# Optimization experiments

Measured on AMD Instinct MI355X. Metric: run time of the kernel, lower is better.

## Reference

```python
import jax, jax.numpy as jnp
import numpy as np

NEG = -9e15
EPS = 1e-5

# GraphAttention (classic GAT layer): h = xW; e_ij = LeakyReLU(a1.h_i + a2.h_j);
# attention = softmax(where(adj>0, e, -9e15)); out = attention @ h.
# The torch code builds one big block-diagonal adjacency; off-block entries get
# -9e15 and underflow to exactly 0 after softmax, so batched per-block GAT is
# numerically identical and avoids the O((B*N)^2) dense waste.

def gat(x, adj, W, a1, a2):
    h = jnp.einsum('bnf,fh->bnh', x, W)
    e = jax.nn.leaky_relu(jnp.einsum('bnh,h->bn', h, a1)[:, :, None]
                          + jnp.einsum('bnh,h->bn', h, a2)[:, None, :], 0.2)
    att = jax.nn.softmax(jnp.where(adj > 0, e, NEG), axis=-1)
    return jnp.einsum('bnm,bmh->bnh', att, h)

def mlp(x, W1, b1, W2, b2):
    return jax.nn.relu(x @ W1 + b1) @ W2 + b2


def setup_inputs() -> dict:
    key = jax.random.key(0)
    ks = iter(jax.random.split(key, 40))
    B, NV, NO = 8, 500, 1500
    DV, DO, H = 512, 32, 128

    def mat(din, dout):
        return jax.random.normal(next(ks), (din, dout), jnp.float32) / np.sqrt(din)

    def vec(d):
        return jax.random.normal(next(ks), (d,), jnp.float32) * 0.1

    inp = {
        'vis_memory': jax.random.normal(next(ks), (B, NV, DV), jnp.float32),
        'obj_memory': jax.random.normal(next(ks), (B, NO, DO), jnp.float32),
        'vis_adj': jax.random.uniform(next(ks), (B, NV, NV), jnp.float32),
        'obj_adj': jax.random.uniform(next(ks), (B, NO, NO), jnp.float32),
        'object_A_OV': jax.random.uniform(next(ks), (B, NO, NV), jnp.float32),
        # GAT layers
        'Wv1': mat(DV, H), 'av1a': vec(H), 'av1b': vec(H),
        'Wv2': mat(H, H),  'av2a': vec(H), 'av2b': vec(H),
        'Wo1': mat(DO, H), 'ao1a': vec(H), 'ao1b': vec(H),
        'Wo2': mat(H, H),  'ao2a': vec(H), 'ao2b': vec(H),
        # globalTobject / objectTglobal MLPs
        'g2o_W1': mat(H, H), 'g2o_b1': jnp.zeros((H,), jnp.float32),
        'g2o_W2': mat(H, H), 'g2o_b2': jnp.zeros((H,), jnp.float32),
        'o2g_W1': mat(H, H), 'o2g_b1': jnp.zeros((H,), jnp.float32),
        'o2g_W2': mat(H, H), 'o2g_b2': jnp.zeros((H,), jnp.float32),
        # output projections
        'img_W': mat(H, DV), 'img_b': jnp.zeros((DV,), jnp.float32),
        'obj_W': mat(H, DO), 'obj_b': jnp.zeros((DO,), jnp.float32),
    }
    return inp


def reference(vis_memory, obj_memory, vis_adj, obj_adj, object_A_OV,
              Wv1, av1a, av1b, Wv2, av2a, av2b,
              Wo1, ao1a, ao1b, Wo2, ao2a, ao2b,
              g2o_W1, g2o_b1, g2o_W2, g2o_b2,
              o2g_W1, o2g_b1, o2g_W2, o2g_b2,
              img_W, img_b, obj_W, obj_b):
    # cross adjacencies (block-diagonal in torch -> batched here)
    vo = jnp.swapaxes(object_A_OV, 1, 2)            # (B, NV, NO)
    vo = vo / (vo.sum(2, keepdims=True) + EPS)
    ov = jnp.swapaxes(vo, 1, 2)                     # (B, NO, NV)
    ov = ov / (ov.sum(2, keepdims=True) + EPS)

    v1 = jax.nn.relu(gat(vis_memory, vis_adj, Wv1, av1a, av1b))
    o1 = jax.nn.relu(gat(obj_memory, obj_adj, Wo1, ao1a, ao1b))
    vis = v1 + mlp(jnp.einsum('bvo,boh->bvh', vo, o1), o2g_W1, o2g_b1, o2g_W2, o2g_b2)
    obj = o1 + mlp(jnp.einsum('bov,bvh->boh', ov, v1), g2o_W1, g2o_b1, g2o_W2, g2o_b2)

    v2 = jax.nn.relu(gat(vis, vis_adj, Wv2, av2a, av2b))
    o2 = jax.nn.relu(gat(obj, obj_adj, Wo2, ao2a, ao2b))
    vis = v2 + mlp(jnp.einsum('bvo,boh->bvh', vo, o2), o2g_W1, o2g_b1, o2g_W2, o2g_b2)
    obj = o2 + mlp(jnp.einsum('bov,bvh->boh', ov, v2), g2o_W1, g2o_b1, g2o_W2, g2o_b2)

    vis_out = vis @ img_W + img_b                   # (B, NV, DV)
    obj_out = obj @ obj_W + obj_b                   # (B, NO, DO)
    return (vis_out, obj_out)
```

## Files before the change

kernel.cpp:

```cpp
#include <hip/hip_runtime.h>
#include <math.h>

#define EPSV 1e-5f
#define HD 128
#define IT 64
#define JT 32
#define WP 68
#define CCH 16
#define THR 256

typedef __attribute__((address_space(3))) uint32_t lds_u32_t;
typedef __attribute__((address_space(1))) uint32_t gbl_u32_t;
typedef __attribute__((ext_vector_type(8))) short bf16x8;
typedef __attribute__((ext_vector_type(4))) float f32x4;

__device__ __forceinline__ void async_copy16(const float* g, float* l) {
    __builtin_amdgcn_global_load_lds((const gbl_u32_t*)g, (lds_u32_t*)l, 16, 0, 0);
}

__device__ __forceinline__ void stage_tile_async(const float* gsrc, float* lds, int t) {
    int wv = t >> 6, lane = t & 63;
#pragma unroll
    for (int it = 0; it < 4; ++it) {
        int c = it * 4 + wv;
        async_copy16(gsrc + c * 256 + lane * 4, lds + c * 256);
    }
}

__device__ __forceinline__ void stage_8k(const void* g, void* l, int t) {
    const float* gf = (const float*)g; float* lf = (float*)l;
    async_copy16(gf + t * 4, lf + t * 4);
    async_copy16(gf + t * 4 + 1024, lf + t * 4 + 1024);
}

__device__ __forceinline__ unsigned int f2bf(float f) {
    return __builtin_bit_cast(unsigned int, f) >> 16;
}

__device__ __forceinline__ unsigned short rne_bf16(float f) {
    unsigned int u = __builtin_bit_cast(unsigned int, f);
    u += 0x7FFFu + ((u >> 16) & 1u);
    return (unsigned short)(u >> 16);
}

struct WprepP { const float *W, *a1, *a2; unsigned short* WT; float *wa1, *wa2; int K; };
struct XprepP { const float* X; unsigned short* Xbf; const float *wa1, *wa2;
                float *sa, *sb; int rows; };
struct GmfP   { const unsigned short *Xbf, *WT; unsigned short* hT; int N, tilesJ; };
struct MaskP  { const float* adj; unsigned int* maskT; int N, tilesJ, chunks; };
struct AggP  { const unsigned int* mask; const float *sa, *sb, *sm; const unsigned short* hT;
               float *pp, *zp; int N, tiles, tilesJ, tps; };
struct CrossP{ const float *A, *src, *rs1; float *pp; int iN, jN, tiles, tps; };
struct FinP  { const float *pp, *zp; float *out; int rows, S; };
struct MlpP  { const float *pp, *scale; int S; const float *W1, *b1, *W2, *b2, *res;
               float *out; int rows; };


__global__ void colsum_part_k(const float* __restrict__ A, float* __restrict__ s1p,
                              int B, int NO, int NV) {
    int v = blockIdx.x * 256 + threadIdx.x;
    int c = blockIdx.y, b = blockIdx.z;
    if (v >= NV) return;
    int chunk = (NO + CCH - 1) / CCH;
    int o0 = c * chunk;
    int o1 = o0 + chunk; if (o1 > NO) o1 = NO;
    const float* Ab = A + (size_t)b * NO * NV + v;
    float s = 0.f;
    for (int o = o0; o < o1; ++o) s += Ab[(size_t)o * NV];
    s1p[((size_t)b * CCH + c) * NV + v] = s;
}

__global__ void colsum_fin_k(const float* __restrict__ s1p, float* __restrict__ rs1,
                             int B, int NV) {
    int idx = blockIdx.x * 256 + threadIdx.x;
    if (idx >= B * NV) return;
    int b = idx / NV, v = idx - b * NV;
    float s = 0.f;
    for (int c = 0; c < CCH; ++c) s += s1p[((size_t)b * CCH + c) * NV + v];
    rs1[idx] = 1.f / (s + EPSV);
}

__global__ void rowsum_inv_k(const float* __restrict__ A, const float* __restrict__ rs1,
                             float* __restrict__ rs2, int B, int NO, int NV) {
    int row = blockIdx.x * (blockDim.x >> 6) + (threadIdx.x >> 6);
    int lane = threadIdx.x & 63;
    if (row >= B * NO) return;
    int b = row / NO;
    const float* Ar = A + (size_t)row * NV;
    const float* r1 = rs1 + (size_t)b * NV;
    float s = 0.f;
    for (int v = lane; v < NV; v += 64) s += Ar[v] * r1[v];
    for (int off = 32; off; off >>= 1) s += __shfl_xor(s, off, 64);
    if (lane == 0) rs2[row] = 1.f / (s + EPSV);
}

__global__ __launch_bounds__(256)
void mask2_k(MaskP V, MaskP O, int GV) {
    int bid = blockIdx.x;
    const MaskP& P = (bid < GV) ? V : O;
    int lb = (bid < GV) ? bid : bid - GV;
    int t = threadIdx.x;
    int wid = lb * 4 + (t >> 6), lane = t & 63;
    int N = P.N, chunks = P.chunks, tilesJ = P.tilesJ;
    int row = wid / chunks;
    int ch = wid - row * chunks;
    if (row >= 8 * N) return;
    int b = row / N, i = row - b * N;
    int j = ch * 64 + lane;
    float v = (j < N) ? P.adj[(size_t)row * N + j] : 0.f;
    unsigned long long m = __ballot(v > 0.f);
    size_t base = (size_t)b * tilesJ * N;
    int w0 = ch * 2;
    if (lane == 0)                      P.maskT[base + (size_t)w0 * N + i] = (unsigned int)m;
    if (lane == 32 && w0 + 1 < tilesJ)  P.maskT[base + (size_t)(w0 + 1) * N + i] = (unsigned int)(m >> 32);
}

__global__ __launch_bounds__(256)
void wprep_k(WprepP p0, WprepP p1, WprepP p2, WprepP p3, int e0, int e1, int e2) {
    __shared__ float lw[32][129];
    __shared__ float a1s[128], a2s[128];
    int bid = blockIdx.x;
    const WprepP& P = bid < e0 ? p0 : bid < e1 ? p1 : bid < e2 ? p2 : p3;
    int lb = bid < e0 ? bid : bid < e1 ? bid - e0 : bid < e2 ? bid - e1 : bid - e2;
    int k0 = lb * 32, K = P.K;
    int t = threadIdx.x;
    if (t < 128) { a1s[t] = P.a1[t]; a2s[t] = P.a2[t]; }
    for (int idx = t; idx < 32 * 32; idx += 256) {
        int kk = idx >> 5, c4 = idx & 31;
        float4 v = ((const float4*)(P.W + (size_t)(k0 + kk) * 128))[c4];
        lw[kk][c4 * 4 + 0] = v.x; lw[kk][c4 * 4 + 1] = v.y;
        lw[kk][c4 * 4 + 2] = v.z; lw[kk][c4 * 4 + 3] = v.w;
    }
    __syncthreads();
    int kk = t >> 3, g = t & 7;
    float s1 = 0.f, s2 = 0.f;
    for (int c = g; c < 128; c += 8) {
        float w = lw[kk][c];
        s1 = fmaf(w, a1s[c], s1);
        s2 = fmaf(w, a2s[c], s2);
    }
    s1 += __shfl_xor(s1, 1, 64); s1 += __shfl_xor(s1, 2, 64); s1 += __shfl_xor(s1, 4, 64);
    s2 += __shfl_xor(s2, 1, 64); s2 += __shfl_xor(s2, 2, 64); s2 += __shfl_xor(s2, 4, 64);
    if (g == 0) { P.wa1[k0 + kk] = s1; P.wa2[k0 + kk] = s2; }
    for (int idx = t; idx < 4096; idx += 256) {
        int c = idx >> 5, k = idx & 31;
        P.WT[(size_t)c * K + k0 + k] = rne_bf16(lw[k][c]);
    }
}

template<int K>
__device__ void xprep_body(const XprepP& P, int lb) {
    int t = threadIdx.x, wv = t >> 6, lane = t & 63;
    int row = lb * 4 + wv;
    if (row >= P.rows) return;
    const float4* x4 = (const float4*)(P.X + (size_t)row * K);
    const float4* w14 = (const float4*)P.wa1;
    const float4* w24 = (const float4*)P.wa2;
    unsigned short* xb = P.Xbf + (size_t)row * K;
    float s1 = 0.f, s2 = 0.f;
    constexpr int K4 = K / 4;
    constexpr int NI = (K4 + 63) / 64;
#pragma unroll
    for (int i = 0; i < NI; ++i) {
        int k4 = i * 64 + lane;
        if ((K4 % 64 == 0) || (k4 < K4)) {
            float4 x = x4[k4];
            float4 a = w14[k4];
            float4 b = w24[k4];
            s1 += x.x * a.x + x.y * a.y + x.z * a.z + x.w * a.w;
            s2 += x.x * b.x + x.y * b.y + x.z * b.z + x.w * b.w;
            ushort4 p = make_ushort4(rne_bf16(x.x), rne_bf16(x.y),
                                     rne_bf16(x.z), rne_bf16(x.w));
            *(ushort4*)(xb + (size_t)k4 * 4) = p;
        }
    }
#pragma unroll
    for (int off = 32; off; off >>= 1) {
        s1 += __shfl_xor(s1, off, 64);
        s2 += __shfl_xor(s2, off, 64);
    }
    if (lane == 0) { P.sa[row] = s1; P.sb[row] = s2; }
}

template<int KV, int KO>
__global__ __launch_bounds__(256)
void xprep2_k(XprepP V, XprepP O, int GV) {
    int bid = blockIdx.x;
    if (bid < GV) xprep_body<KV>(V, bid);
    else          xprep_body<KO>(O, bid - GV);
}

template<int K>
__device__ void gmf_body(const GmfP& P, int lb) {
    int tilesJ = P.tilesJ, N = P.N;
    int b = lb / tilesJ, jt = lb - b * tilesJ;
    int t = threadIdx.x, wv = t >> 6, lane = t & 63;
    int ml = lane & 15, quad = lane >> 4;
    const unsigned short* xb = P.Xbf + ((size_t)b * N + (size_t)jt * 32) * K;
    const unsigned short* wt0 = P.WT + (size_t)(wv * 32 + ml) * K;
    const unsigned short* wt1 = wt0 + (size_t)16 * K;
    const unsigned short* xb0 = xb + (size_t)ml * K;
    const unsigned short* xb1 = xb + (size_t)(16 + ml) * K;
    f32x4 acc00 = {0.f, 0.f, 0.f, 0.f}, acc01 = acc00, acc10 = acc00, acc11 = acc00;
#pragma unroll 4
    for (int kt = 0; kt < K / 32; ++kt) {
        int kk = kt * 32 + quad * 8;
        bf16x8 a0 = *(const bf16x8*)(wt0 + kk);
        bf16x8 a1 = *(const bf16x8*)(wt1 + kk);
        bf16x8 b0 = *(const bf16x8*)(xb0 + kk);
        bf16x8 b1 = *(const bf16x8*)(xb1 + kk);
        acc00 = __builtin_amdgcn_mfma_f32_16x16x32_bf16(a0, b0, acc00, 0, 0, 0);
        acc01 = __builtin_amdgcn_mfma_f32_16x16x32_bf16(a0, b1, acc01, 0, 0, 0);
        acc10 = __builtin_amdgcn_mfma_f32_16x16x32_bf16(a1, b0, acc10, 0, 0, 0);
        acc11 = __builtin_amdgcn_mfma_f32_16x16x32_bf16(a1, b1, acc11, 0, 0, 0);
    }
    unsigned short* hb = P.hT + (size_t)(b * tilesJ + jt) * 4096;
    int nvalid = N - jt * 32; if (nvalid > 32) nvalid = 32;
    bool ok0 = ml < nvalid, ok1 = (16 + ml) < nvalid;
    int c0 = wv * 32 + quad * 4;
#pragma unroll
    for (int r = 0; r < 4; ++r) {
        int ca = c0 + r, cb = c0 + 16 + r;
        int swa = ((ca >> 1) & 3) << 3, swb = ((cb >> 1) & 3) << 3;
        hb[ca * 32 + (ml ^ swa)]        = ok0 ? rne_bf16(acc00[r]) : 0;
        hb[ca * 32 + ((16 + ml) ^ swa)] = ok1 ? rne_bf16(acc01[r]) : 0;
        hb[cb * 32 + (ml ^ swb)]        = ok0 ? rne_bf16(acc10[r]) : 0;
        hb[cb * 32 + ((16 + ml) ^ swb)] = ok1 ? rne_bf16(acc11[r]) : 0;
    }
}

template<int KV, int KO>
__global__ __launch_bounds__(256)
void gmf2_k(GmfP V, GmfP O, int GV) {
    int bid = blockIdx.x;
    if (bid < GV) gmf_body<KV>(V, bid);
    else          gmf_body<KO>(O, bid - GV);
}

__global__ __launch_bounds__(256)
void sbmax2_k(const float* __restrict__ sbV, float* __restrict__ smV,
              const float* __restrict__ sbO, float* __restrict__ smO,
              int NV, int NO) {
    __shared__ float red[256];
    int b0 = blockIdx.x, t = threadIdx.x;
    const float* sb; float* out; int N;
    if (b0 < 8) { sb = sbV + (size_t)b0 * NV; out = smV + b0; N = NV; }
    else        { sb = sbO + (size_t)(b0 - 8) * NO; out = smO + (b0 - 8); N = NO; }
    float m = -INFINITY;
    for (int j = t; j < N; j += 256) m = fmaxf(m, sb[j]);
    red[t] = m; __syncthreads();
    for (int s = 128; s; s >>= 1) {
        if (t < s) red[t] = fmaxf(red[t], red[t + s]);
        __syncthreads();
    }
    if (t == 0) *out = red[0];
}

struct SharedAggM {
    unsigned short hsT[3][128][32];
    unsigned short wsA[2][4][64][8];
    unsigned int mask_s[12][64];
    float sb_s[12 * 32];
    float sa_s[IT], m_s[IT];
};

__device__ void agg_body(SharedAggM& sm, const AggP& P, int lbid) {
    int tiles = P.tiles;
    int split = lbid / (8 * tiles);
    int rem = lbid - split * 8 * tiles;
    int b = rem / tiles;
    int i0 = (rem - b * tiles) * IT;
    int N = P.N;
    int jt0 = split * P.tps;
    if (jt0 >= P.tilesJ) return;
    int jt1 = jt0 + P.tps; if (jt1 > P.tilesJ) jt1 = P.tilesJ;
    int T = jt1 - jt0;
    int t = threadIdx.x;
    if (t < IT) {
        int i = i0 + t;
        float s = (i < N) ? P.sa[(size_t)b * N + i] : 0.f;
        sm.sa_s[t] = s;
        float e = s + P.sm[b];
        sm.m_s[t] = e > 0.f ? e : 0.2f * e;
    }
    for (int idx = t; idx < (T << 6); idx += 256) {
        int w = idx >> 6, r = idx & 63;
        int ir = i0 + r;
        sm.mask_s[w][r] = (ir < N)
            ? P.mask[((size_t)b * P.tilesJ + jt0 + w) * N + ir] : 0u;
    }
    const float* sbb = P.sb + (size_t)b * N;
    for (int idx = t; idx < (T << 5); idx += 256) {
        int j = (jt0 << 5) + idx;
        sm.sb_s[idx] = (j < N) ? sbb[j] : 0.f;
    }
    __syncthreads();
    const unsigned short* hTb = P.hT + ((size_t)b * P.tilesJ + jt0) * 4096;
    stage_8k(hTb, &sm.hsT[0][0][0], t);
    if (T > 1) stage_8k(hTb + 4096, &sm.hsT[1][0][0], t);

    int wv = t >> 6, lane = t & 63;
    int il = t >> 2, j4 = (t & 3) * 4;
    int q0 = j4 >> 3, i0w = j4 & 7, wrow = il & 15;
    int nquad = lane >> 4, nlow = lane & 15;
    int nq2 = (nquad ^ ((nlow >> 1) & 3)) * 8;
    f32x4 acc[8];
#pragma unroll
    for (int nt = 0; nt < 8; ++nt)
#pragma unroll
        for (int r = 0; r < 4; ++r) acc[nt][r] = 0.f;
    float zacc = 0.f;
    int irow = i0 + il;
    const float4* sb4 = (const float4*)sm.sb_s;
    for (int tt = 0; tt < T; ++tt) {
        int cur = tt - (tt / 3) * 3;
        unsigned int mw = sm.mask_s[tt][il];
        float4 sA = sb4[tt * 8 + (t & 3)];
        float4 sB = sb4[tt * 8 + (t & 3) + 4];
        float sai = sm.sa_s[il], m = sm.m_s[il];
#pragma unroll
        for (int k = 0; k < 2; ++k) {
            float sv[4];
            { float4 s4 = k ? sB : sA; sv[0] = s4.x; sv[1] = s4.y; sv[2] = s4.z; sv[3] = s4.w; }
            float w_[4];
#pragma unroll
            for (int r = 0; r < 4; ++r) {
                float e = sai + sv[r];
                e = e > 0.f ? e : 0.2f * e;
                float ww = __expf(e - m);
                ww = ((mw >> (j4 + k * 16 + r)) & 1u) ? ww : 0.f;
                zacc += ww;
                w_[r] = ww;
            }
            unsigned int lo = f2bf(w_[0]) | (__builtin_bit_cast(unsigned int, w_[1]) & 0xFFFF0000u);
            unsigned int hi = f2bf(w_[2]) | (__builtin_bit_cast(unsigned int, w_[3]) & 0xFFFF0000u);
            *(uint2*)&sm.wsA[tt & 1][wv][wrow + 16 * (q0 + 2 * k)][i0w] = make_uint2(lo, hi);
        }
        if (tt + 1 < T) asm volatile("s_waitcnt vmcnt(2) lgkmcnt(0)" ::: "memory");
        else            asm volatile("s_waitcnt vmcnt(0) lgkmcnt(0)" ::: "memory");
        __builtin_amdgcn_s_barrier();
        asm volatile("" ::: "memory");
        if (tt + 2 < T) {
            int nb = tt + 2; nb -= (nb / 3) * 3;
            stage_8k(hTb + (size_t)(tt + 2) * 4096, &sm.hsT[nb][0][0], t);
        }
        bf16x8 afrag = *(const bf16x8*)&sm.wsA[tt & 1][wv][lane][0];
#pragma unroll
        for (int nt = 0; nt < 8; ++nt) {
            bf16x8 bfrag = *(const bf16x8*)&sm.hsT[cur][nt * 16 + nlow][nq2];
            acc[nt] = __builtin_amdgcn_mfma_f32_16x16x32_bf16(afrag, bfrag, acc[nt], 0, 0, 0);
        }
    }
    zacc += __shfl_xor(zacc, 1, 64);
    zacc += __shfl_xor(zacc, 2, 64);
    size_t rowsTot = (size_t)8 * N;
    float* pp = P.pp + ((size_t)split * rowsTot + (size_t)b * N) * HD;
#pragma unroll
    for (int nt = 0; nt < 8; ++nt)
#pragma unroll
        for (int r = 0; r < 4; ++r) {
            int row = i0 + wv * 16 + nquad * 4 + r;
            if (row < N) pp[(size_t)row * HD + nt * 16 + nlow] = acc[nt][r];
        }
    if ((t & 3) == 0 && irow < N)
        P.zp[(size_t)split * rowsTot + (size_t)b * N + irow] = zacc;
}

__global__ __launch_bounds__(256)
void agg2_k(AggP V, AggP O, int GVb) {
    __shared__ SharedAggM sm;
    int bid = blockIdx.x;
    if (bid < GVb) agg_body(sm, V, bid);
    else           agg_body(sm, O, bid - GVb);
}

__device__ __forceinline__ void tile_fma256(const float (*hs)[HD], const float (*ws)[WP],
                                            int rg, int c0, float acc[4][8]) {
#pragma unroll 8
    for (int jl = 0; jl < JT; ++jl) {
        float4 h0 = *(const float4*)&hs[jl][c0];
        float4 h1 = *(const float4*)&hs[jl][c0 + 64];
        float4 w4 = *(const float4*)&ws[jl][rg * 4];
        float wq[4] = {w4.x, w4.y, w4.z, w4.w};
#pragma unroll
        for (int q = 0; q < 4; ++q) {
            float w = wq[q];
            acc[q][0] = fmaf(w, h0.x, acc[q][0]);
            acc[q][1] = fmaf(w, h0.y, acc[q][1]);
            acc[q][2] = fmaf(w, h0.z, acc[q][2]);
            acc[q][3] = fmaf(w, h0.w, acc[q][3]);
            acc[q][4] = fmaf(w, h1.x, acc[q][4]);
            acc[q][5] = fmaf(w, h1.y, acc[q][5]);
            acc[q][6] = fmaf(w, h1.z, acc[q][6]);
            acc[q][7] = fmaf(w, h1.w, acc[q][7]);
        }
    }
}

__device__ __forceinline__ void part_store256(float* __restrict__ pp, size_t base,
                                              int i0, int N, int rg, int c0,
                                              float acc[4][8]) {
#pragma unroll
    for (int q = 0; q < 4; ++q) {
        int i = i0 + rg * 4 + q;
        if (i >= N) continue;
        float* op = pp + base + (size_t)i * HD;
        *(float4*)&op[c0]      = make_float4(acc[q][0], acc[q][1], acc[q][2], acc[q][3]);
        *(float4*)&op[c0 + 64] = make_float4(acc[q][4], acc[q][5], acc[q][6], acc[q][7]);
    }
}

struct SharedTile { float hs[2][JT][HD]; float ws[2][JT][WP]; };

__device__ void cross_vo_body(SharedTile& sm, const CrossP& P, int lbid) {
    int tiles = P.tiles;
    int split = lbid / (8 * tiles);
    int rem = lbid - split * 8 * tiles;
    int b = rem / tiles;
    int i0 = (rem - b * tiles) * IT;
    int NVl = P.iN, NOl = P.jN;
    int j_begin = split * P.tps * JT;
    if (j_begin >= NOl) return;
    int j_end = j_begin + P.tps * JT;
    if (j_end > NOl) j_end = NOl;
    int T = (j_end - j_begin + JT - 1) / JT;
    int t = threadIdx.x;
    int rg = t >> 4, c0 = (t & 15) * 4;
    int il = t & 63, jlb = t >> 6;
    float acc[4][8];
#pragma unroll
    for (int q = 0; q < 4; ++q)
#pragma unroll
        for (int x = 0; x < 8; ++x) acc[q][x] = 0.f;
    const float* Ab = P.A + (size_t)b * NOl * NVl;
    const float* srcb = P.src + (size_t)b * NOl * HD;
    int v = i0 + il;
    float w8[8];
    stage_tile_async(srcb + (size_t)j_begin * HD, &sm.hs[0][0][0], t);
#pragma unroll
    for (int k = 0; k < 8; ++k) {
        int o = j_begin + jlb + k * 4;
        w8[k] = (v < NVl && o < NOl) ? Ab[(size_t)o * NVl + v] : 0.f;
    }
    for (int tt = 0; tt < T; ++tt) {
        int cur = tt & 1;
#pragma unroll
        for (int k = 0; k < 8; ++k) sm.ws[cur][jlb + k * 4][il] = w8[k];
        __syncthreads();
        if (tt + 1 < T) {
            int jn = j_begin + (tt + 1) * JT;
            stage_tile_async(srcb + (size_t)jn * HD, &sm.hs[1 - cur][0][0], t);
#pragma unroll
            for (int k = 0; k < 8; ++k) {
                int o = jn + jlb + k * 4;
                w8[k] = (v < NVl && o < NOl) ? Ab[(size_t)o * NVl + v] : 0.f;
            }
        }
        tile_fma256(sm.hs[cur], sm.ws[cur], rg, c0, acc);
    }
    size_t rowsTot = (size_t)8 * NVl;
    part_store256(P.pp, ((size_t)split * rowsTot + (size_t)b * NVl) * HD, i0, NVl, rg, c0, acc);
}

__device__ void cross_ov_body(SharedTile& sm, const CrossP& P, int lbid) {
    int tiles = P.tiles;
    int split = lbid / (8 * tiles);
    int rem = lbid - split * 8 * tiles;
    int b = rem / tiles;
    int i0 = (rem - b * tiles) * IT;
    int NOl = P.iN, NVl = P.jN;
    int j_begin = split * P.tps * JT;
    if (j_begin >= NVl) return;
    int j_end = j_begin + P.tps * JT;
    if (j_end > NVl) j_end = NVl;
    int T = (j_end - j_begin + JT - 1) / JT;
    int t = threadIdx.x;
    int rg = t >> 4, c0 = (t & 15) * 4;
    int il = t >> 2, j4 = (t & 3) * 4;
    float acc[4][8];
#pragma unroll
    for (int q = 0; q < 4; ++q)
#pragma unroll
        for (int x = 0; x < 8; ++x) acc[q][x] = 0.f;
    const float* Ab = P.A + (size_t)b * NOl * NVl;
    const float* srcb = P.src + (size_t)b * NVl * HD;
    const float* r1b = P.rs1 + (size_t)b * NVl;
    int orow = i0 + il;
    float4 a4[2], r4[2];
    stage_tile_async(srcb + (size_t)j_begin * HD, &sm.hs[0][0][0], t);
#pragma unroll
    for (int k = 0; k < 2; ++k) {
        int vv = j_begin + j4 + k * 16;
        float4 av = make_float4(0.f,0.f,0.f,0.f), rv = make_float4(0.f,0.f,0.f,0.f);
        if (orow < NOl) {
            if (vv + 3 < NVl) {
                av = *(const float4*)&Ab[(size_t)orow * NVl + vv];
                rv = *(const float4*)&r1b[vv];
            } else {
                float* ap = (float*)&av; float* rp = (float*)&rv;
                for (int r = 0; r < 4; ++r)
                    if (vv + r < NVl) { ap[r] = Ab[(size_t)orow * NVl + vv + r]; rp[r] = r1b[vv + r]; }
            }
        }
        a4[k] = av; r4[k] = rv;
    }
    for (int tt = 0; tt < T; ++tt) {
        int cur = tt & 1;
#pragma unroll
        for (int k = 0; k < 2; ++k) {
            float wv[4] = {a4[k].x * r4[k].x, a4[k].y * r4[k].y,
                           a4[k].z * r4[k].z, a4[k].w * r4[k].w};
#pragma unroll
            for (int r = 0; r < 4; ++r) sm.ws[cur][j4 + r + k * 16][il] = wv[r];
        }
        __syncthreads();
        if (tt + 1 < T) {
            int jn = j_begin + (tt + 1) * JT;
            stage_tile_async(srcb + (size_t)jn * HD, &sm.hs[1 - cur][0][0], t);
#pragma unroll
            for (int k = 0; k < 2; ++k) {
                int vv = jn + j4 + k * 16;
                float4 av = make_float4(0.f,0.f,0.f,0.f), rv = make_float4(0.f,0.f,0.f,0.f);
                if (orow < NOl) {
                    if (vv + 3 < NVl) {
                        av = *(const float4*)&Ab[(size_t)orow * NVl + vv];
                        rv = *(const float4*)&r1b[vv];
                    } else {
                        float* ap = (float*)&av; float* rp = (float*)&rv;
                        for (int r = 0; r < 4; ++r)
                            if (vv + r < NVl) { ap[r] = Ab[(size_t)orow * NVl + vv + r]; rp[r] = r1b[vv + r]; }
                    }
                }
                a4[k] = av; r4[k] = rv;
            }
        }
        tile_fma256(sm.hs[cur], sm.ws[cur], rg, c0, acc);
    }
    size_t rowsTot = (size_t)8 * NOl;
    part_store256(P.pp, ((size_t)split * rowsTot + (size_t)b * NOl) * HD, i0, NOl, rg, c0, acc);
}

__global__ __launch_bounds__(256)
void cross2_k(CrossP VO, CrossP OV, int GVOb) {
    __shared__ SharedTile sm;
    int bid = blockIdx.x;
    if (bid < GVOb) cross_vo_body(sm, VO, bid);
    else            cross_ov_body(sm, OV, bid - GVOb);
}

__global__ __launch_bounds__(256)
void fin2_k(FinP V, FinP O, int GVb) {
    int bid = blockIdx.x;
    const FinP& P = (bid < GVb) ? V : O;
    int idx = ((bid < GVb) ? bid : bid - GVb) * 256 + threadIdx.x;
    int rows = P.rows;
    int row = idx >> 5;
    if (row >= rows) return;
    float4 v = make_float4(0.f, 0.f, 0.f, 0.f);
    for (int s = 0; s < P.S; ++s) {
        float4 p = ((const float4*)P.pp)[((size_t)s * rows + row) * 32 + (idx & 31)];
        v.x += p.x; v.y += p.y; v.z += p.z; v.w += p.w;
    }
    float z = 0.f;
    for (int s = 0; s < P.S; ++s) z += P.zp[(size_t)s * rows + row];
    float sc = 1.f / z;
    v.x = fmaxf(v.x * sc, 0.f); v.y = fmaxf(v.y * sc, 0.f);
    v.z = fmaxf(v.z * sc, 0.f); v.w = fmaxf(v.w * sc, 0.f);
    ((float4*)P.out)[idx] = v;
}

__global__ __launch_bounds__(128)
void mlp2_k(MlpP V, MlpP O, int GVb) {
    __shared__ float xs[8][HD];
    __shared__ float hh[8][HD];
    int bid = blockIdx.x;
    const MlpP& P = (bid < GVb) ? V : O;
    int row0 = ((bid < GVb) ? bid : bid - GVb) * 8;
    int rows = P.rows;
    int t = threadIdx.x;
    for (int l = t; l < 8 * 32; l += 128) {
        int r = l >> 5, c4 = l & 31;
        int row = row0 + r;
        float4 v = make_float4(0.f, 0.f, 0.f, 0.f);
        if (row < rows) {
            for (int s = 0; s < P.S; ++s) {
                float4 p = ((const float4*)P.pp)[((size_t)s * rows + row) * 32 + c4];
                v.x += p.x; v.y += p.y; v.z += p.z; v.w += p.w;
            }
            float sc = P.scale[row];
            v.x *= sc; v.y *= sc; v.z *= sc; v.w *= sc;
        }
        ((float4*)&xs[r][0])[c4] = v;
    }
    __syncthreads();
    int wv = t >> 6, tt = t & 63, rb = wv * 4;
    float a0[4] = {0.f, 0.f, 0.f, 0.f}, a1v[4] = {0.f, 0.f, 0.f, 0.f};
#pragma unroll 4
    for (int k = 0; k < HD; ++k) {
        float w0 = P.W1[(size_t)k * HD + tt];
        float w1 = P.W1[(size_t)k * HD + tt + 64];
#pragma unroll
        for (int r = 0; r < 4; ++r) {
            float x = xs[rb + r][k];
            a0[r] = fmaf(x, w0, a0[r]);
            a1v[r] = fmaf(x, w1, a1v[r]);
        }
    }
    float bb0 = P.b1[tt], bb1 = P.b1[tt + 64];
#pragma unroll
    for (int r = 0; r < 4; ++r) {
        hh[rb + r][tt]      = fmaxf(a0[r] + bb0, 0.f);
        hh[rb + r][tt + 64] = fmaxf(a1v[r] + bb1, 0.f);
    }
    __syncthreads();
    float c0a[4] = {0.f, 0.f, 0.f, 0.f}, c1a[4] = {0.f, 0.f, 0.f, 0.f};
#pragma unroll 4
    for (int k = 0; k < HD; ++k) {
        float w0 = P.W2[(size_t)k * HD + tt];
        float w1 = P.W2[(size_t)k * HD + tt + 64];
#pragma unroll
        for (int r = 0; r < 4; ++r) {
            float x = hh[rb + r][k];
            c0a[r] = fmaf(x, w0, c0a[r]);
            c1a[r] = fmaf(x, w1, c1a[r]);
        }
    }
    float d0 = P.b2[tt], d1 = P.b2[tt + 64];
#pragma unroll
    for (int r = 0; r < 4; ++r) {
        int row = row0 + rb + r;
        if (row >= rows) continue;
        P.out[(size_t)row * HD + tt]      = c0a[r] + d0 + P.res[(size_t)row * HD + tt];
        P.out[(size_t)row * HD + tt + 64] = c1a[r] + d1 + P.res[(size_t)row * HD + tt + 64];
    }
}

template<int RELU, int BIAS, int RES>
__global__ __launch_bounds__(128)
void linear_k(const float* __restrict__ X, const float* __restrict__ W,
              const float* __restrict__ bias, const float* __restrict__ res,
              float* __restrict__ out, int rows, int K, int Dout) {
    __shared__ float xs[4][512];
    int row0 = blockIdx.x * 4;
    int t = threadIdx.x;
    int K4 = K >> 2;
    for (int l = t; l < 4 * K4; l += 128) {
        int r = l / K4, c4 = l - r * K4;
        float4 val = make_float4(0.f, 0.f, 0.f, 0.f);
        if (row0 + r < rows) val = ((const float4*)(X + (size_t)(row0 + r) * K))[c4];
        ((float4*)&xs[r][0])[c4] = val;
    }
    __syncthreads();
    int chunk = Dout < 256 ? Dout : 256;
    int half = chunk >> 1;
    if (t >= half) return;
    int c0 = blockIdx.y * chunk + t;
    int c1 = c0 + half;
    float a00 = 0, a01 = 0, a02 = 0, a03 = 0, a10 = 0, a11 = 0, a12 = 0, a13 = 0;
#pragma unroll 4
    for (int k = 0; k < K; ++k) {
        float w0 = W[(size_t)k * Dout + c0];
        float w1 = W[(size_t)k * Dout + c1];
        float x0 = xs[0][k], x1 = xs[1][k], x2 = xs[2][k], x3 = xs[3][k];
        a00 = fmaf(x0, w0, a00); a01 = fmaf(x1, w0, a01);
        a02 = fmaf(x2, w0, a02); a03 = fmaf(x3, w0, a03);
        a10 = fmaf(x0, w1, a10); a11 = fmaf(x1, w1, a11);
        a12 = fmaf(x2, w1, a12); a13 = fmaf(x3, w1, a13);
    }
    float accs[2][4] = {{a00, a01, a02, a03}, {a10, a11, a12, a13}};
    int cs[2] = {c0, c1};
    for (int h = 0; h < 2; ++h) {
        float bv = BIAS ? bias[cs[h]] : 0.f;
        for (int r = 0; r < 4; ++r) {
            int row = row0 + r;
            if (row >= rows) continue;
            float v = accs[h][r] + bv;
            if (RES) v += res[(size_t)row * Dout + cs[h]];
            if (RELU) v = fmaxf(v, 0.f);
            out[(size_t)row * Dout + cs[h]] = v;
        }
    }
}

extern "C" void kernel_launch(void* const* d_in, const int* in_sizes, int n_in,
                              void* d_out, int out_size, void* d_ws, size_t ws_size,
                              hipStream_t stream) {
    const int B = 8, NV = 500, NO = 1500, DV = 512, DO = 32;
    const float* vis_memory = (const float*)d_in[0];
    const float* obj_memory = (const float*)d_in[1];
    const float* vis_adj    = (const float*)d_in[2];
    const float* obj_adj    = (const float*)d_in[3];
    const float* A_OV       = (const float*)d_in[4];
    const float* Wv1  = (const float*)d_in[5];
    const float* av1a = (const float*)d_in[6];
    const float* av1b = (const float*)d_in[7];
    const float* Wv2  = (const float*)d_in[8];
    const float* av2a = (const float*)d_in[9];
    const float* av2b = (const float*)d_in[10];
    const float* Wo1  = (const float*)d_in[11];
    const float* ao1a = (const float*)d_in[12];
    const float* ao1b = (const float*)d_in[13];
    const float* Wo2  = (const float*)d_in[14];
    const float* ao2a = (const float*)d_in[15];
    const float* ao2b = (const float*)d_in[16];
    const float* g2o_W1 = (const float*)d_in[17];
    const float* g2o_b1 = (const float*)d_in[18];
    const float* g2o_W2 = (const float*)d_in[19];
    const float* g2o_b2 = (const float*)d_in[20];
    const float* o2g_W1 = (const float*)d_in[21];
    const float* o2g_b1 = (const float*)d_in[22];
    const float* o2g_W2 = (const float*)d_in[23];
    const float* o2g_b2 = (const float*)d_in[24];
    const float* img_W = (const float*)d_in[25];
    const float* img_b = (const float*)d_in[26];
    const float* obj_W = (const float*)d_in[27];
    const float* obj_b = (const float*)d_in[28];

    const int tilesJV = 16, tilesJO = 47;

    float* wsp = (float*)d_ws;
    size_t off = 0;
    auto alloc = [&](size_t n) { float* p = wsp + off; off += (n + 3) & ~(size_t)3; return p; };
    float* rs1   = alloc(B * NV);
    float* rs2   = alloc(B * NO);
    float* saV   = alloc(B * NV);
    float* sbV   = alloc(B * NV);
    float* smV   = alloc(B);
    float* saO   = alloc(B * NO);
    float* sbO   = alloc(B * NO);
    float* smO   = alloc(B);
    float* s1p   = alloc((size_t)B * CCH * NV);
    unsigned int* maskV = (unsigned int*)alloc((size_t)B * tilesJV * NV);
    unsigned int* maskO = (unsigned int*)alloc((size_t)B * tilesJO * NO);
    unsigned short* WTv1 = (unsigned short*)alloc(128 * 512 / 2);
    unsigned short* WTo1 = (unsigned short*)alloc(128 * 32 / 2);
    unsigned short* WTv2 = (unsigned short*)alloc(128 * 128 / 2);
    unsigned short* WTo2 = (unsigned short*)alloc(128 * 128 / 2);
    float* wav1a = alloc(512); float* wav1b = alloc(512);
    float* wao1a = alloc(32);  float* wao1b = alloc(32);
    float* wav2a = alloc(128); float* wav2b = alloc(128);
    float* wao2a = alloc(128); float* wao2b = alloc(128);
    unsigned short* XbfV = (unsigned short*)alloc((size_t)B * NV * 512 / 2);
    unsigned short* XbfO = (unsigned short*)alloc((size_t)B * NO * 128 / 2);
    unsigned short* hTv = (unsigned short*)alloc((size_t)B * tilesJV * 4096 / 2);
    unsigned short* hTo = (unsigned short*)alloc((size_t)B * tilesJO * 4096 / 2);
    float* v1    = alloc((size_t)B * NV * HD);
    float* o1    = alloc((size_t)B * NO * HD);
    float* visb  = alloc((size_t)B * NV * HD);
    float* objb  = alloc((size_t)B * NO * HD);
    float* ppV   = alloc((size_t)8 * B * NV * HD);
    float* zpV   = alloc((size_t)8 * B * NV);
    float* ppO   = alloc((size_t)4 * B * NO * HD);
    float* zpO   = alloc((size_t)4 * B * NO);
    alloc(16384);

    {
        WprepP w0{Wv1, av1a, av1b, WTv1, wav1a, wav1b, DV};
        WprepP w1{Wo1, ao1a, ao1b, WTo1, wao1a, wao1b, DO};
        WprepP w2{Wv2, av2a, av2b, WTv2, wav2a, wav2b, HD};
        WprepP w3{Wo2, ao2a, ao2b, WTo2, wao2a, wao2b, HD};
        wprep_k<<<25, 256, 0, stream>>>(w0, w1, w2, w3, 16, 17, 21);
    }
    {
        const int chunksV = (NV + 63) / 64;
        const int chunksO = (NO + 63) / 64;
        const int G_MSK_V = B * NV * chunksV / 4;
        const int G_MSK_O = B * NO * chunksO / 4;
        MaskP mv{vis_adj, maskV, NV, tilesJV, chunksV};
        MaskP mo{obj_adj, maskO, NO, tilesJO, chunksO};
        mask2_k<<<G_MSK_V + G_MSK_O, 256, 0, stream>>>(mv, mo, G_MSK_V);
    }

    colsum_part_k<<<dim3((NV + 255) / 256, CCH, B), 256, 0, stream>>>(A_OV, s1p, B, NO, NV);
    colsum_fin_k<<<dim3((B * NV + 255) / 256), 256, 0, stream>>>(s1p, rs1, B, NV);
    rowsum_inv_k<<<dim3((B * NO + 3) / 4), 256, 0, stream>>>(A_OV, rs1, rs2, B, NO, NV);

    const int tilesV = 8, tilesO = 24;
    const int SV = 8, SO = 4, SVO = 8, SOV = 4;
    const int tpsV = 2;
    const int tpsO = 12;
    const int tpsVO = 6;
    const int tpsOV = 4;
    const int G_AGG_V = B * tilesV * SV;
    const int G_AGG_O = B * tilesO * SO;
    const int G_CR_VO = B * tilesV * SVO;
    const int G_CR_OV = B * tilesO * SOV;
    const int G_MLP_V = B * NV / 8;
    const int G_MLP_O = B * NO / 8;
    const int G_FIN_V = B * NV * 32 / 256;
    const int G_FIN_O = B * NO * 32 / 256;
    const int G_XP_V = B * NV / 4;
    const int G_XP_O = B * NO / 4;
    const int G_GMF_V = B * tilesJV;
    const int G_GMF_O = B * tilesJO;

    auto tail = [&](float* visout, float* objout) {
        sbmax2_k<<<16, 256, 0, stream>>>(sbV, smV, sbO, smO, NV, NO);
        AggP av{maskV, saV, sbV, smV, hTv, ppV, zpV, NV, tilesV, tilesJV, tpsV};
        AggP ao{maskO, saO, sbO, smO, hTo, ppO, zpO, NO, tilesO, tilesJO, tpsO};
        agg2_k<<<G_AGG_V + G_AGG_O, THR, 0, stream>>>(av, ao, G_AGG_V);
        FinP fv{ppV, zpV, v1, B * NV, SV};
        FinP fo{ppO, zpO, o1, B * NO, SO};
        fin2_k<<<G_FIN_V + G_FIN_O, 256, 0, stream>>>(fv, fo, G_FIN_V);
        CrossP cvo{A_OV, o1, nullptr, ppV, NV, NO, tilesV, tpsVO};
        CrossP cov{A_OV, v1, rs1, ppO, NO, NV, tilesO, tpsOV};
        cross2_k<<<G_CR_VO + G_CR_OV, THR, 0, stream>>>(cvo, cov, G_CR_VO);
        MlpP mv{ppV, rs1, SVO, o2g_W1, o2g_b1, o2g_W2, o2g_b2, v1, visout, B * NV};
        MlpP mo{ppO, rs2, SOV, g2o_W1, g2o_b1, g2o_W2, g2o_b2, o1, objout, B * NO};
        mlp2_k<<<G_MLP_V + G_MLP_O, 128, 0, stream>>>(mv, mo, G_MLP_V);
    };

    {
        XprepP xv{vis_memory, XbfV, wav1a, wav1b, saV, sbV, B * NV};
        XprepP xo{obj_memory, XbfO, wao1a, wao1b, saO, sbO, B * NO};
        xprep2_k<512, 32><<<G_XP_V + G_XP_O, 256, 0, stream>>>(xv, xo, G_XP_V);
        GmfP gv{XbfV, WTv1, hTv, NV, tilesJV};
        GmfP go{XbfO, WTo1, hTo, NO, tilesJO};
        gmf2_k<512, 32><<<G_GMF_V + G_GMF_O, 256, 0, stream>>>(gv, go, G_GMF_V);
        tail(visb, objb);
    }
    {
        XprepP xv{visb, XbfV, wav2a, wav2b, saV, sbV, B * NV};
        XprepP xo{objb, XbfO, wao2a, wao2b, saO, sbO, B * NO};
        xprep2_k<128, 128><<<G_XP_V + G_XP_O, 256, 0, stream>>>(xv, xo, G_XP_V);
        GmfP gv{XbfV, WTv2, hTv, NV, tilesJV};
        GmfP go{XbfO, WTo2, hTo, NO, tilesJO};
        gmf2_k<128, 128><<<G_GMF_V + G_GMF_O, 256, 0, stream>>>(gv, go, G_GMF_V);
        tail(visb, objb);
    }

    float* vis_out = (float*)d_out;
    float* obj_out = vis_out + (size_t)B * NV * DV;
    linear_k<0, 1, 0><<<dim3((B * NV + 3) / 4, (DV + 255) / 256), 128, 0, stream>>>(
        visb, img_W, img_b, nullptr, vis_out, B * NV, HD, DV);
    linear_k<0, 1, 0><<<dim3((B * NO + 3) / 4, 1), 128, 0, stream>>>(
        objb, obj_W, obj_b, nullptr, obj_out, B * NO, HD, DO);
}
```

Measured before the change: 623.3 us.

## Drop split-K in GAT aggregation, fuse normalization, rewrite adjacency mask kernel

The aggregation kernel no longer splits the neighbour dimension across blocks. Each block now loops over all J tiles, keeps the softmax denominator in shared memory, and writes the normalized, ReLU'd output directly. This removes the partial-sum buffers and the separate finalize kernel launch along with its global round trip. The mask build changes from a wave-ballot kernel to one thread per 32-bit word, reading float4s, with separate templated launches for the vis and obj adjacencies. In exchange the aggregation grid shrinks several-fold, to about one block per CU, with longer serial loops per block, so latency hiding and parallelism may suffer.

New measurement: 634.4 us. Within noise of the previous version (+1.8%).

```diff
diff --git a/kernel.cpp b/kernel.cpp
--- a/kernel.cpp
+++ b/kernel.cpp
@@ -47,11 +47,9 @@
 struct XprepP { const float* X; unsigned short* Xbf; const float *wa1, *wa2;
                 float *sa, *sb; int rows; };
 struct GmfP   { const unsigned short *Xbf, *WT; unsigned short* hT; int N, tilesJ; };
-struct MaskP  { const float* adj; unsigned int* maskT; int N, tilesJ, chunks; };
 struct AggP  { const unsigned int* mask; const float *sa, *sb, *sm; const unsigned short* hT;
-               float *pp, *zp; int N, tiles, tilesJ, tps; };
+               float* out; int N, tiles, tilesJ; };
 struct CrossP{ const float *A, *src, *rs1; float *pp; int iN, jN, tiles, tps; };
-struct FinP  { const float *pp, *zp; float *out; int rows, S; };
 struct MlpP  { const float *pp, *scale; int S; const float *W1, *b1, *W2, *b2, *res;
                float *out; int rows; };
 
@@ -94,25 +92,32 @@
     if (lane == 0) rs2[row] = 1.f / (s + EPSV);
 }
 
+template<int N, int TILESJ>
 __global__ __launch_bounds__(256)
-void mask2_k(MaskP V, MaskP O, int GV) {
-    int bid = blockIdx.x;
-    const MaskP& P = (bid < GV) ? V : O;
-    int lb = (bid < GV) ? bid : bid - GV;
-    int t = threadIdx.x;
-    int wid = lb * 4 + (t >> 6), lane = t & 63;
-    int N = P.N, chunks = P.chunks, tilesJ = P.tilesJ;
-    int row = wid / chunks;
-    int ch = wid - row * chunks;
-    if (row >= 8 * N) return;
-    int b = row / N, i = row - b * N;
-    int j = ch * 64 + lane;
-    float v = (j < N) ? P.adj[(size_t)row * N + j] : 0.f;
-    unsigned long long m = __ballot(v > 0.f);
-    size_t base = (size_t)b * tilesJ * N;
-    int w0 = ch * 2;
-    if (lane == 0)                      P.maskT[base + (size_t)w0 * N + i] = (unsigned int)m;
-    if (lane == 32 && w0 + 1 < tilesJ)  P.maskT[base + (size_t)(w0 + 1) * N + i] = (unsigned int)(m >> 32);
+void maskg_k(const float* __restrict__ adj, unsigned int* __restrict__ maskT) {
+    int tid = blockIdx.x * 256 + threadIdx.x;
+    int w = tid % TILESJ;
+    int rowid = tid / TILESJ;
+    if (rowid >= 8 * N) return;
+    int b = rowid / N, i = rowid - b * N;
+    int j0 = w * 32;
+    const float* src = adj + (size_t)rowid * N + j0;
+    unsigned int bits = 0u;
+    if (j0 + 32 <= N) {
+#pragma unroll
+        for (int q = 0; q < 8; ++q) {
+            float4 v = ((const float4*)src)[q];
+            bits |= (v.x > 0.f ? 1u : 0u) << (q * 4 + 0);
+            bits |= (v.y > 0.f ? 1u : 0u) << (q * 4 + 1);
+            bits |= (v.z > 0.f ? 1u : 0u) << (q * 4 + 2);
+            bits |= (v.w > 0.f ? 1u : 0u) << (q * 4 + 3);
+        }
+    } else {
+#pragma unroll
+        for (int r = 0; r < 32; ++r)
+            if (j0 + r < N) bits |= (src[r] > 0.f ? 1u : 0u) << r;
+    }
+    maskT[((size_t)b * TILESJ + w) * N + i] = bits;
 }
 
 __global__ __launch_bounds__(256)
@@ -259,22 +264,17 @@
 struct SharedAggM {
     unsigned short hsT[3][128][32];
     unsigned short wsA[2][4][64][8];
-    unsigned int mask_s[12][64];
-    float sb_s[12 * 32];
-    float sa_s[IT], m_s[IT];
+    unsigned int mask_s[48][64];
+    float sb_s[48 * 32];
+    float sa_s[IT], m_s[IT], z_s[IT];
 };
 
 __device__ void agg_body(SharedAggM& sm, const AggP& P, int lbid) {
     int tiles = P.tiles;
-    int split = lbid / (8 * tiles);
-    int rem = lbid - split * 8 * tiles;
-    int b = rem / tiles;
-    int i0 = (rem - b * tiles) * IT;
+    int b = lbid / tiles;
+    int i0 = (lbid - b * tiles) * IT;
     int N = P.N;
-    int jt0 = split * P.tps;
-    if (jt0 >= P.tilesJ) return;
-    int jt1 = jt0 + P.tps; if (jt1 > P.tilesJ) jt1 = P.tilesJ;
-    int T = jt1 - jt0;
+    int T = P.tilesJ;
     int t = threadIdx.x;
     if (t < IT) {
         int i = i0 + t;
@@ -287,17 +287,16 @@
         int w = idx >> 6, r = idx & 63;
         int ir = i0 + r;
         sm.mask_s[w][r] = (ir < N)
-            ? P.mask[((size_t)b * P.tilesJ + jt0 + w) * N + ir] : 0u;
+            ? P.mask[((size_t)b * T + w) * N + ir] : 0u;
     }
     const float* sbb = P.sb + (size_t)b * N;
     for (int idx = t; idx < (T << 5); idx += 256) {
-        int j = (jt0 << 5) + idx;
-        sm.sb_s[idx] = (j < N) ? sbb[j] : 0.f;
+        sm.sb_s[idx] = (idx < N) ? sbb[idx] : 0.f;
     }
     __syncthreads();
-    const unsigned short* hTb = P.hT + ((size_t)b * P.tilesJ + jt0) * 4096;
+    const unsigned short* hTb = P.hT + (size_t)b * T * 4096;
     stage_8k(hTb, &sm.hsT[0][0][0], t);
-    if (T > 1) stage_8k(hTb + 4096, &sm.hsT[1][0][0], t);
+    stage_8k(hTb + 4096, &sm.hsT[1][0][0], t);
 
     int wv = t >> 6, lane = t & 63;
     int il = t >> 2, j4 = (t & 3) * 4;
@@ -310,7 +309,6 @@
 #pragma unroll
         for (int r = 0; r < 4; ++r) acc[nt][r] = 0.f;
     float zacc = 0.f;
-    int irow = i0 + il;
     const float4* sb4 = (const float4*)sm.sb_s;
     for (int tt = 0; tt < T; ++tt) {
         int cur = tt - (tt / 3) * 3;
@@ -353,17 +351,20 @@
     }
     zacc += __shfl_xor(zacc, 1, 64);
     zacc += __shfl_xor(zacc, 2, 64);
-    size_t rowsTot = (size_t)8 * N;
-    float* pp = P.pp + ((size_t)split * rowsTot + (size_t)b * N) * HD;
+    if ((t & 3) == 0) sm.z_s[il] = zacc;
+    __syncthreads();
+    float inv[4];
+#pragma unroll
+    for (int r = 0; r < 4; ++r) inv[r] = 1.f / sm.z_s[wv * 16 + nquad * 4 + r];
+    float* outb = P.out + (size_t)b * N * HD;
 #pragma unroll
     for (int nt = 0; nt < 8; ++nt)
 #pragma unroll
         for (int r = 0; r < 4; ++r) {
             int row = i0 + wv * 16 + nquad * 4 + r;
-            if (row < N) pp[(size_t)row * HD + nt * 16 + nlow] = acc[nt][r];
-        }
-    if ((t & 3) == 0 && irow < N)
-        P.zp[(size_t)split * rowsTot + (size_t)b * N + irow] = zacc;
+            if (row < N)
+                outb[(size_t)row * HD + nt * 16 + nlow] = fmaxf(acc[nt][r] * inv[r], 0.f);
+        }
 }
 
 __global__ __launch_bounds__(256)
@@ -546,27 +547,6 @@
     int bid = blockIdx.x;
     if (bid < GVOb) cross_vo_body(sm, VO, bid);
     else            cross_ov_body(sm, OV, bid - GVOb);
-}
-
-__global__ __launch_bounds__(256)
-void fin2_k(FinP V, FinP O, int GVb) {
-    int bid = blockIdx.x;
-    const FinP& P = (bid < GVb) ? V : O;
-    int idx = ((bid < GVb) ? bid : bid - GVb) * 256 + threadIdx.x;
-    int rows = P.rows;
-    int row = idx >> 5;
-    if (row >= rows) return;
-    float4 v = make_float4(0.f, 0.f, 0.f, 0.f);
-    for (int s = 0; s < P.S; ++s) {
-        float4 p = ((const float4*)P.pp)[((size_t)s * rows + row) * 32 + (idx & 31)];
-        v.x += p.x; v.y += p.y; v.z += p.z; v.w += p.w;
-    }
-    float z = 0.f;
-    for (int s = 0; s < P.S; ++s) z += P.zp[(size_t)s * rows + row];
-    float sc = 1.f / z;
-    v.x = fmaxf(v.x * sc, 0.f); v.y = fmaxf(v.y * sc, 0.f);
-    v.z = fmaxf(v.z * sc, 0.f); v.w = fmaxf(v.w * sc, 0.f);
-    ((float4*)P.out)[idx] = v;
 }
 
 __global__ __launch_bounds__(128)
@@ -749,9 +729,7 @@
     float* visb  = alloc((size_t)B * NV * HD);
     float* objb  = alloc((size_t)B * NO * HD);
     float* ppV   = alloc((size_t)8 * B * NV * HD);
-    float* zpV   = alloc((size_t)8 * B * NV);
     float* ppO   = alloc((size_t)4 * B * NO * HD);
-    float* zpO   = alloc((size_t)4 * B * NO);
     alloc(16384);
 
     {
@@ -761,34 +739,23 @@
         WprepP w3{Wo2, ao2a, ao2b, WTo2, wao2a, wao2b, HD};
         wprep_k<<<25, 256, 0, stream>>>(w0, w1, w2, w3, 16, 17, 21);
     }
-    {
-        const int chunksV = (NV + 63) / 64;
-        const int chunksO = (NO + 63) / 64;
-        const int G_MSK_V = B * NV * chunksV / 4;
-        const int G_MSK_O = B * NO * chunksO / 4;
-        MaskP mv{vis_adj, maskV, NV, tilesJV, chunksV};
-        MaskP mo{obj_adj, maskO, NO, tilesJO, chunksO};
-        mask2_k<<<G_MSK_V + G_MSK_O, 256, 0, stream>>>(mv, mo, G_MSK_V);
-    }
+    maskg_k<500, 16><<<(8 * 500 * 16 + 255) / 256, 256, 0, stream>>>(vis_adj, maskV);
+    maskg_k<1500, 47><<<(8 * 1500 * 47 + 255) / 256, 256, 0, stream>>>(obj_adj, maskO);
 
     colsum_part_k<<<dim3((NV + 255) / 256, CCH, B), 256, 0, stream>>>(A_OV, s1p, B, NO, NV);
     colsum_fin_k<<<dim3((B * NV + 255) / 256), 256, 0, stream>>>(s1p, rs1, B, NV);
     rowsum_inv_k<<<dim3((B * NO + 3) / 4), 256, 0, stream>>>(A_OV, rs1, rs2, B, NO, NV);
 
     const int tilesV = 8, tilesO = 24;
-    const int SV = 8, SO = 4, SVO = 8, SOV = 4;
-    const int tpsV = 2;
-    const int tpsO = 12;
+    const int SVO = 8, SOV = 4;
     const int tpsVO = 6;
     const int tpsOV = 4;
-    const int G_AGG_V = B * tilesV * SV;
-    const int G_AGG_O = B * tilesO * SO;
+    const int G_AGG_V = B * tilesV;
+    const int G_AGG_O = B * tilesO;
     const int G_CR_VO = B * tilesV * SVO;
     const int G_CR_OV = B * tilesO * SOV;
     const int G_MLP_V = B * NV / 8;
     const int G_MLP_O = B * NO / 8;
-    const int G_FIN_V = B * NV * 32 / 256;
-    const int G_FIN_O = B * NO * 32 / 256;
     const int G_XP_V = B * NV / 4;
     const int G_XP_O = B * NO / 4;
     const int G_GMF_V = B * tilesJV;
@@ -796,12 +763,9 @@
 
     auto tail = [&](float* visout, float* objout) {
         sbmax2_k<<<16, 256, 0, stream>>>(sbV, smV, sbO, smO, NV, NO);
-        AggP av{maskV, saV, sbV, smV, hTv, ppV, zpV, NV, tilesV, tilesJV, tpsV};
-        AggP ao{maskO, saO, sbO, smO, hTo, ppO, zpO, NO, tilesO, tilesJO, tpsO};
+        AggP av{maskV, saV, sbV, smV, hTv, v1, NV, tilesV, tilesJV};
+        AggP ao{maskO, saO, sbO, smO, hTo, o1, NO, tilesO, tilesJO};
         agg2_k<<<G_AGG_V + G_AGG_O, THR, 0, stream>>>(av, ao, G_AGG_V);
-        FinP fv{ppV, zpV, v1, B * NV, SV};
-        FinP fo{ppO, zpO, o1, B * NO, SO};
-        fin2_k<<<G_FIN_V + G_FIN_O, 256, 0, stream>>>(fv, fo, G_FIN_V);
         CrossP cvo{A_OV, o1, nullptr, ppV, NV, NO, tilesV, tpsVO};
         CrossP cov{A_OV, v1, rs1, ppO, NO, NV, tilesO, tpsOV};
         cross2_k<<<G_CR_VO + G_CR_OV, THR, 0, stream>>>(cvo, cov, G_CR_VO);
```
